# Kernel tuning notes

Measured on AMD Instinct MI355X. Metric: run time of the kernel, lower is better.

## Reference

```python
import jax, jax.numpy as jnp
import numpy as np

N, D, E, OUT = 100000, 128, 600000, 128


def setup_inputs() -> dict:
    key = jax.random.key(0)
    k1, k2, k3, k4, k5 = jax.random.split(key, 5)
    x = jax.random.normal(k1, (N, D), dtype=jnp.float32)
    # Linear params (stored as [in, out]; y = h @ W + b, same math as nn.Linear)
    W = jax.random.normal(k2, (D, OUT), dtype=jnp.float32) * (1.0 / np.sqrt(D))
    b = jax.random.normal(k3, (OUT,), dtype=jnp.float32) * 0.01
    # Flattened ragged neighbor lists as COO edges: node edge_dst[e] aggregates x[edge_src[e]]
    edge_src = jax.random.randint(k4, (E,), 0, N, dtype=jnp.int32)
    edge_dst = jnp.sort(jax.random.randint(k5, (E,), 0, N, dtype=jnp.int32))
    return {"x": x, "W": W, "b": b, "edge_src": edge_src, "edge_dst": edge_dst}


def reference(x, W, b, edge_src, edge_dst):
    n = x.shape[0]
    # segment-mean of neighbor features per destination node
    neigh_sum = jax.ops.segment_sum(x[edge_src], edge_dst, num_segments=n)  # [N, D]
    deg = jax.ops.segment_sum(jnp.ones((edge_dst.shape[0],), x.dtype), edge_dst, num_segments=n)  # [N]
    # nodes with no neighbors keep zero mean (matches `if neigh:` branch)
    neigh_mean = neigh_sum / jnp.maximum(deg, 1.0)[:, None]
    h = x + neigh_mean
    return jax.nn.relu(h @ W + b)
```

## Files before the change

### kernel.cpp

```cpp
#include <hip/hip_runtime.h>
#include <hip/hip_bf16.h>


#define FD  128
#define BR  64
#define HSB 136

typedef __attribute__((ext_vector_type(8))) short bf16x8;
typedef __attribute__((ext_vector_type(4))) float f32x4;

__device__ __forceinline__ short f2bf(float f) {
    unsigned u = __float_as_uint(f);
    unsigned r = (u + 0x7FFFu + ((u >> 16) & 1u)) >> 16;
    return (short)r;
}

__global__ __launch_bounds__(256) void prep_kernel(
    const float* __restrict__ W, const int* __restrict__ edst,
    int* __restrict__ rp, short* __restrict__ pkW, int N, int E)
{
    int gid = blockIdx.x * 256 + threadIdx.x;
    if (gid < E) {
        int cur = edst[gid];
        int prev = gid ? edst[gid - 1] : -1;
        for (int v = prev + 1; v <= cur; ++v) rp[v] = gid;
        if (gid == E - 1)
            for (int v = cur + 1; v <= N; ++v) rp[v] = E;
    }
    if (gid < 2048) {
        int wave = gid >> 9, rem = gid & 511;
        int ct = rem >> 8, rem2 = rem & 255;
        int kt = rem2 >> 6, lane = rem2 & 63;
        int q = lane >> 4, lr = lane & 15;
        int col = wave * 32 + ct * 16 + lr;
        int k0 = kt * 32 + q * 8;
        short tmp[8];
#pragma unroll
        for (int e = 0; e < 8; ++e)
            tmp[e] = f2bf(W[(size_t)(k0 + e) * FD + col]);
        *(bf16x8*)(pkW + (size_t)gid * 8) = *(bf16x8*)tmp;
    }
}

__global__ __launch_bounds__(256) void meanagg_main_kernel(
    const float* __restrict__ x, const short* __restrict__ pkW,
    const float* __restrict__ bias, const int* __restrict__ esrc,
    const int* __restrict__ rp, float* __restrict__ out, int N, int E)
{
    __shared__ short shb[BR * HSB];
    __shared__ int seg[BR + 1];

    const int t = threadIdx.x;
    const int base = blockIdx.x * BR;

    if (t < BR + 1) {
        int idx = base + t;
        seg[t] = rp[idx > N ? N : idx];
    }
    __syncthreads();

    const int wave = t >> 6;
    const int lane = t & 63;
    const int sw = lane >> 5;
    const int sl = lane & 31;
    const int lb = sw << 5;
    const int rowbase = wave * 16;

    {
        int rb0 = rowbase + sw;
        int r0  = base + rb0;
        int s0  = (r0 < N) ? seg[rb0] : 0;
        int e0  = (r0 < N) ? seg[rb0 + 1] : 0;
        int src_next = (s0 + sl < e0) ? esrc[s0 + sl] : 0;
        float4 xv_next = make_float4(0.f, 0.f, 0.f, 0.f);
        if (r0 < N) xv_next = *(const float4*)(x + (size_t)r0 * FD + 4 * sl);

        int s = s0, e = e0;
        for (int it = 0; it < 8; ++it) {
            const int cur_rb = rowbase + it * 2 + sw;
            const int cur_r  = base + cur_rb;
            const int cur_s  = s, cur_e = e;
            const int src_l  = src_next;
            const float4 xv  = xv_next;

            if (it < 7) {
                int nrb = rowbase + (it + 1) * 2 + sw;
                int nr  = base + nrb;
                s = (nr < N) ? seg[nrb] : 0;
                e = (nr < N) ? seg[nrb + 1] : 0;
                src_next = (s + sl < e) ? esrc[s + sl] : 0;
                xv_next = make_float4(0.f, 0.f, 0.f, 0.f);
                if (nr < N) xv_next = *(const float4*)(x + (size_t)nr * FD + 4 * sl);
            }

            if (cur_r < N) {
                float4 a0 = make_float4(0.f, 0.f, 0.f, 0.f), a1 = a0;
                int srcv = src_l;
                for (int cs = cur_s; cs < cur_e; cs += 32) {
                    int m = cur_e - cs; if (m > 32) m = 32;
                    if (cs != cur_s)
                        srcv = (cs + sl < cur_e) ? esrc[cs + sl] : 0;
                    for (int j0 = 0; j0 < m; j0 += 8) {
                        const int rem = m - j0;
                        float4 v[8];
#pragma unroll
                        for (int u = 0; u < 8; ++u) {
                            int idx = __shfl(srcv, lb + ((j0 + u) & 31));
                            v[u] = *(const float4*)(x + (size_t)idx * FD + 4 * sl);
                        }
#pragma unroll
                        for (int u = 0; u < 8; ++u) {
                            float f = (u < rem) ? 1.f : 0.f;
                            float4* A = (u & 1) ? &a1 : &a0;
                            A->x = fmaf(v[u].x, f, A->x);
                            A->y = fmaf(v[u].y, f, A->y);
                            A->z = fmaf(v[u].z, f, A->z);
                            A->w = fmaf(v[u].w, f, A->w);
                        }
                    }
                }
                int deg = cur_e - cur_s;
                float inv = 1.0f / (float)(deg > 0 ? deg : 1);
                short4 hb;
                hb.x = f2bf(xv.x + (a0.x + a1.x) * inv);
                hb.y = f2bf(xv.y + (a0.y + a1.y) * inv);
                hb.z = f2bf(xv.z + (a0.z + a1.z) * inv);
                hb.w = f2bf(xv.w + (a0.w + a1.w) * inv);
                *(short4*)(shb + cur_rb * HSB + 4 * sl) = hb;
            }
        }
    }
    __syncthreads();

    const int lr = lane & 15;
    const int q  = lane >> 4;
    const int colb = wave * 32;

    bf16x8 bfr[2][4];
#pragma unroll
    for (int ct = 0; ct < 2; ++ct)
#pragma unroll
        for (int kt = 0; kt < 4; ++kt) {
            int f = ((wave * 2 + ct) * 4 + kt) * 64 + lane;
            bfr[ct][kt] = *(const bf16x8*)(pkW + (size_t)f * 8);
        }

    f32x4 acc[4][2];
#pragma unroll
    for (int rt = 0; rt < 4; ++rt) {
        acc[rt][0] = (f32x4){0.f, 0.f, 0.f, 0.f};
        acc[rt][1] = (f32x4){0.f, 0.f, 0.f, 0.f};
    }

#pragma unroll
    for (int rt = 0; rt < 4; ++rt)
#pragma unroll
        for (int kt = 0; kt < 4; ++kt) {
            bf16x8 a = *(const bf16x8*)(shb + (rt * 16 + lr) * HSB + kt * 32 + q * 8);
            acc[rt][0] = __builtin_amdgcn_mfma_f32_16x16x32_bf16(a, bfr[0][kt], acc[rt][0], 0, 0, 0);
            acc[rt][1] = __builtin_amdgcn_mfma_f32_16x16x32_bf16(a, bfr[1][kt], acc[rt][1], 0, 0, 0);
        }

    const float b0 = bias[colb + lr];
    const float b1 = bias[colb + 16 + lr];

#pragma unroll
    for (int rt = 0; rt < 4; ++rt)
#pragma unroll
        for (int j = 0; j < 4; ++j) {
            int row = base + rt * 16 + q * 4 + j;
            if (row < N) {
                float v0 = acc[rt][0][j] + b0; v0 = v0 > 0.f ? v0 : 0.f;
                float v1 = acc[rt][1][j] + b1; v1 = v1 > 0.f ? v1 : 0.f;
                out[(size_t)row * FD + colb + lr]      = v0;
                out[(size_t)row * FD + colb + 16 + lr] = v1;
            }
        }
}

__global__ __launch_bounds__(256) void meanagg_fused_kernel(
    const float* __restrict__ x, const float* __restrict__ W,
    const float* __restrict__ bias, const int* __restrict__ esrc,
    const int* __restrict__ edst, float* __restrict__ out, int N, int E)
{
    __shared__ short shb[BR * HSB];
    __shared__ int seg[BR + 1];

    const int t = threadIdx.x;
    const int base = blockIdx.x * BR;

    if (t < BR + 1) {
        int v = base + t;
        int lo = 0, hi = E;
        while (lo < hi) {
            int mid = (lo + hi) >> 1;
            if (edst[mid] < v) lo = mid + 1; else hi = mid;
        }
        seg[t] = lo;
    }
    __syncthreads();

    const int wave = t >> 6;
    const int lane = t & 63;
    const int sw = lane >> 5;
    const int sl = lane & 31;
    const int lb = sw << 5;
    const int rowbase = wave * 16;

    {
        int rb0 = rowbase + sw;
        int r0  = base + rb0;
        int s0  = (r0 < N) ? seg[rb0] : 0;
        int e0  = (r0 < N) ? seg[rb0 + 1] : 0;
        int src_next = (s0 + sl < e0) ? esrc[s0 + sl] : 0;
        float4 xv_next = make_float4(0.f, 0.f, 0.f, 0.f);
        if (r0 < N) xv_next = *(const float4*)(x + (size_t)r0 * FD + 4 * sl);

        int s = s0, e = e0;
        for (int it = 0; it < 8; ++it) {
            const int cur_rb = rowbase + it * 2 + sw;
            const int cur_r  = base + cur_rb;
            const int cur_s  = s, cur_e = e;
            const int src_l  = src_next;
            const float4 xv  = xv_next;

            if (it < 7) {
                int nrb = rowbase + (it + 1) * 2 + sw;
                int nr  = base + nrb;
                s = (nr < N) ? seg[nrb] : 0;
                e = (nr < N) ? seg[nrb + 1] : 0;
                src_next = (s + sl < e) ? esrc[s + sl] : 0;
                xv_next = make_float4(0.f, 0.f, 0.f, 0.f);
                if (nr < N) xv_next = *(const float4*)(x + (size_t)nr * FD + 4 * sl);
            }

            if (cur_r < N) {
                float4 a0 = make_float4(0.f, 0.f, 0.f, 0.f), a1 = a0;
                int srcv = src_l;
                for (int cs = cur_s; cs < cur_e; cs += 32) {
                    int m = cur_e - cs; if (m > 32) m = 32;
                    if (cs != cur_s)
                        srcv = (cs + sl < cur_e) ? esrc[cs + sl] : 0;
                    for (int j0 = 0; j0 < m; j0 += 8) {
                        const int rem = m - j0;
                        float4 v[8];
#pragma unroll
                        for (int u = 0; u < 8; ++u) {
                            int idx = __shfl(srcv, lb + ((j0 + u) & 31));
                            v[u] = *(const float4*)(x + (size_t)idx * FD + 4 * sl);
                        }
#pragma unroll
                        for (int u = 0; u < 8; ++u) {
                            float f = (u < rem) ? 1.f : 0.f;
                            float4* A = (u & 1) ? &a1 : &a0;
                            A->x = fmaf(v[u].x, f, A->x);
                            A->y = fmaf(v[u].y, f, A->y);
                            A->z = fmaf(v[u].z, f, A->z);
                            A->w = fmaf(v[u].w, f, A->w);
                        }
                    }
                }
                int deg = cur_e - cur_s;
                float inv = 1.0f / (float)(deg > 0 ? deg : 1);
                short4 hb;
                hb.x = f2bf(xv.x + (a0.x + a1.x) * inv);
                hb.y = f2bf(xv.y + (a0.y + a1.y) * inv);
                hb.z = f2bf(xv.z + (a0.z + a1.z) * inv);
                hb.w = f2bf(xv.w + (a0.w + a1.w) * inv);
                *(short4*)(shb + cur_rb * HSB + 4 * sl) = hb;
            }
        }
    }
    __syncthreads();

    const int lr = lane & 15;
    const int q  = lane >> 4;
    const int colb = wave * 32;

    bf16x8 bfr[2][4];
#pragma unroll
    for (int ct = 0; ct < 2; ++ct) {
        int col = colb + ct * 16 + lr;
#pragma unroll
        for (int kt = 0; kt < 4; ++kt) {
            bf16x8 f;
#pragma unroll
            for (int e = 0; e < 8; ++e)
                f[e] = f2bf(W[(size_t)(kt * 32 + q * 8 + e) * FD + col]);
            bfr[ct][kt] = f;
        }
    }

    f32x4 acc[4][2];
#pragma unroll
    for (int rt = 0; rt < 4; ++rt) {
        acc[rt][0] = (f32x4){0.f, 0.f, 0.f, 0.f};
        acc[rt][1] = (f32x4){0.f, 0.f, 0.f, 0.f};
    }

#pragma unroll
    for (int rt = 0; rt < 4; ++rt)
#pragma unroll
        for (int kt = 0; kt < 4; ++kt) {
            bf16x8 a = *(const bf16x8*)(shb + (rt * 16 + lr) * HSB + kt * 32 + q * 8);
            acc[rt][0] = __builtin_amdgcn_mfma_f32_16x16x32_bf16(a, bfr[0][kt], acc[rt][0], 0, 0, 0);
            acc[rt][1] = __builtin_amdgcn_mfma_f32_16x16x32_bf16(a, bfr[1][kt], acc[rt][1], 0, 0, 0);
        }

    const float b0 = bias[colb + lr];
    const float b1 = bias[colb + 16 + lr];

#pragma unroll
    for (int rt = 0; rt < 4; ++rt)
#pragma unroll
        for (int j = 0; j < 4; ++j) {
            int row = base + rt * 16 + q * 4 + j;
            if (row < N) {
                float v0 = acc[rt][0][j] + b0; v0 = v0 > 0.f ? v0 : 0.f;
                float v1 = acc[rt][1][j] + b1; v1 = v1 > 0.f ? v1 : 0.f;
                out[(size_t)row * FD + colb + lr]      = v0;
                out[(size_t)row * FD + colb + 16 + lr] = v1;
            }
        }
}

extern "C" void kernel_launch(void* const* d_in, const int* in_sizes, int n_in,
                              void* d_out, int out_size, void* d_ws, size_t ws_size,
                              hipStream_t stream) {
    const float* x    = (const float*)d_in[0];
    const float* W    = (const float*)d_in[1];
    const float* bias = (const float*)d_in[2];
    const int* esrc   = (const int*)d_in[3];
    const int* edst   = (const int*)d_in[4];
    float* out        = (float*)d_out;

    int N = in_sizes[0] / FD;
    int E = in_sizes[3];
    int blocks = (N + BR - 1) / BR;

    size_t rp_bytes  = (size_t)(N + 1) * 4;
    size_t pk_off    = (rp_bytes + 511) & ~(size_t)511;
    size_t need      = pk_off + 2048 * 8 * 2;

    if (ws_size >= need) {
        int* rp    = (int*)d_ws;
        short* pkW = (short*)((char*)d_ws + pk_off);
        int pblocks = (E + 255) / 256;
        prep_kernel<<<pblocks, 256, 0, stream>>>(W, edst, rp, pkW, N, E);
        meanagg_main_kernel<<<blocks, 256, 0, stream>>>(x, pkW, bias, esrc, rp, out, N, E);
    } else {
        meanagg_fused_kernel<<<blocks, 256, 0, stream>>>(x, W, bias, esrc, edst, out, N, E);
    }
}
```

Measured before the change: 71.76 us.

## Pre-convert node features to bf16 and gather bf16 rows in aggregation

Adds a prep pass that converts x to bf16 in workspace alongside the CSR row pointers and packed W. A new main kernel gathers neighbor rows as bf16 (16 lanes × 8 values per row) with 6-wide unrolled loads, which halves the bytes moved by the random gather. The cost is an extra full read of x and a write of its bf16 copy each call, plus reduced precision in the aggregated features. The fallback fused kernel is also simplified, dropping its software prefetch.

```diff
diff --git a/kernel.cpp b/kernel.cpp
--- a/kernel.cpp
+++ b/kernel.cpp
@@ -11,8 +11,194 @@
 
 __device__ __forceinline__ short f2bf(float f) {
     unsigned u = __float_as_uint(f);
-    unsigned r = (u + 0x7FFFu + ((u >> 16) & 1u)) >> 16;
-    return (short)r;
+    return (short)((u + 0x7FFFu + ((u >> 16) & 1u)) >> 16);
+}
+__device__ __forceinline__ float bf2f(short s) {
+    return __uint_as_float(((unsigned)(unsigned short)s) << 16);
+}
+
+__global__ __launch_bounds__(256) void prep_full_kernel(
+    const float* __restrict__ x, const float* __restrict__ W,
+    const int* __restrict__ edst, int* __restrict__ rp,
+    short* __restrict__ pkW, short* __restrict__ xb, int N, int E)
+{
+    const int gid = blockIdx.x * 256 + threadIdx.x;
+    const int nth = gridDim.x * 256;
+
+    const int nv = N * FD / 8;
+    for (int i = gid; i < nv; i += nth) {
+        float4 f0 = *(const float4*)(x + (size_t)i * 8);
+        float4 f1 = *(const float4*)(x + (size_t)i * 8 + 4);
+        short tmp[8] = {f2bf(f0.x), f2bf(f0.y), f2bf(f0.z), f2bf(f0.w),
+                        f2bf(f1.x), f2bf(f1.y), f2bf(f1.z), f2bf(f1.w)};
+        *(bf16x8*)(xb + (size_t)i * 8) = *(bf16x8*)tmp;
+    }
+    for (int e = gid; e < E; e += nth) {
+        int cur = edst[e];
+        int prev = e ? edst[e - 1] : -1;
+        for (int v = prev + 1; v <= cur; ++v) rp[v] = e;
+        if (e == E - 1)
+            for (int v = cur + 1; v <= N; ++v) rp[v] = E;
+    }
+    if (gid < 2048) {
+        int wave = gid >> 9, rem = gid & 511;
+        int ct = rem >> 8, rem2 = rem & 255;
+        int kt = rem2 >> 6, lane = rem2 & 63;
+        int q = lane >> 4, lr = lane & 15;
+        int col = wave * 32 + ct * 16 + lr;
+        int k0 = kt * 32 + q * 8;
+        short tmp[8];
+#pragma unroll
+        for (int e2 = 0; e2 < 8; ++e2)
+            tmp[e2] = f2bf(W[(size_t)(k0 + e2) * FD + col]);
+        *(bf16x8*)(pkW + (size_t)gid * 8) = *(bf16x8*)tmp;
+    }
+}
+
+__global__ __launch_bounds__(256) void meanagg_main2_kernel(
+    const short* __restrict__ xb, const short* __restrict__ pkW,
+    const float* __restrict__ bias, const int* __restrict__ esrc,
+    const int* __restrict__ rp, float* __restrict__ out, int N, int E)
+{
+    __shared__ short shb[BR * HSB];
+    __shared__ int seg[BR + 1];
+
+    const int t = threadIdx.x;
+    const int base = blockIdx.x * BR;
+
+    if (t < BR + 1) {
+        int idx = base + t;
+        seg[t] = rp[idx > N ? N : idx];
+    }
+    __syncthreads();
+
+    const int wave = t >> 6;
+    const int lane = t & 63;
+    const int qw = lane >> 4;
+    const int ql = lane & 15;
+    const int qb = qw << 4;
+    const int rowbase = wave * 16;
+
+    {
+        int rb0 = rowbase + qw;
+        int r0  = base + rb0;
+        int s = (r0 < N) ? seg[rb0] : 0;
+        int e = (r0 < N) ? seg[rb0 + 1] : 0;
+        int srcv_n = (s + ql < e) ? esrc[s + ql] : 0;
+        bf16x8 xv_n = {0, 0, 0, 0, 0, 0, 0, 0};
+        if (r0 < N) xv_n = *(const bf16x8*)(xb + (size_t)r0 * FD + 8 * ql);
+
+        for (int it = 0; it < 4; ++it) {
+            const int cur_rb = rowbase + it * 4 + qw;
+            const int cur_r  = base + cur_rb;
+            const int cs0 = s, ce = e;
+            int srcv = srcv_n;
+            const bf16x8 xv = xv_n;
+
+            if (it < 3) {
+                int nrb = rowbase + (it + 1) * 4 + qw;
+                int nr  = base + nrb;
+                s = (nr < N) ? seg[nrb] : 0;
+                e = (nr < N) ? seg[nrb + 1] : 0;
+                srcv_n = (s + ql < e) ? esrc[s + ql] : 0;
+                bf16x8 z = {0, 0, 0, 0, 0, 0, 0, 0};
+                xv_n = z;
+                if (nr < N) xv_n = *(const bf16x8*)(xb + (size_t)nr * FD + 8 * ql);
+            }
+
+            if (cur_r < N) {
+                float a[8];
+#pragma unroll
+                for (int p = 0; p < 8; ++p) a[p] = 0.f;
+
+                for (int cs = cs0; cs < ce; cs += 16) {
+                    int m = ce - cs; if (m > 16) m = 16;
+                    if (cs != cs0)
+                        srcv = (cs + ql < ce) ? esrc[cs + ql] : 0;
+                    for (int j0 = 0; j0 < m; j0 += 6) {
+                        uint4 v[6];
+#pragma unroll
+                        for (int u = 0; u < 6; ++u) {
+                            int jj = j0 + u;
+                            int idx = __shfl(srcv, qb + (jj & 15));
+                            if (jj >= m) idx = 0;
+                            v[u] = *(const uint4*)(xb + (size_t)idx * FD + 8 * ql);
+                        }
+#pragma unroll
+                        for (int u = 0; u < 6; ++u) {
+                            float f = (j0 + u < m) ? 1.f : 0.f;
+                            unsigned w;
+                            w = v[u].x;
+                            a[0] = fmaf(__uint_as_float(w << 16), f, a[0]);
+                            a[1] = fmaf(__uint_as_float(w & 0xFFFF0000u), f, a[1]);
+                            w = v[u].y;
+                            a[2] = fmaf(__uint_as_float(w << 16), f, a[2]);
+                            a[3] = fmaf(__uint_as_float(w & 0xFFFF0000u), f, a[3]);
+                            w = v[u].z;
+                            a[4] = fmaf(__uint_as_float(w << 16), f, a[4]);
+                            a[5] = fmaf(__uint_as_float(w & 0xFFFF0000u), f, a[5]);
+                            w = v[u].w;
+                            a[6] = fmaf(__uint_as_float(w << 16), f, a[6]);
+                            a[7] = fmaf(__uint_as_float(w & 0xFFFF0000u), f, a[7]);
+                        }
+                    }
+                }
+                int deg = ce - cs0;
+                float inv = 1.0f / (float)(deg > 0 ? deg : 1);
+                short hb[8];
+#pragma unroll
+                for (int p = 0; p < 8; ++p)
+                    hb[p] = f2bf(bf2f(xv[p]) + a[p] * inv);
+                *(bf16x8*)(shb + cur_rb * HSB + 8 * ql) = *(bf16x8*)hb;
+            }
+        }
+    }
+    __syncthreads();
+
+    const int lr = lane & 15;
+    const int q  = lane >> 4;
+    const int colb = wave * 32;
+
+    bf16x8 bfr[2][4];
+#pragma unroll
+    for (int ct = 0; ct < 2; ++ct)
+#pragma unroll
+        for (int kt = 0; kt < 4; ++kt) {
+            int f = ((wave * 2 + ct) * 4 + kt) * 64 + lane;
+            bfr[ct][kt] = *(const bf16x8*)(pkW + (size_t)f * 8);
+        }
+
+    f32x4 acc[4][2];
+#pragma unroll
+    for (int rt = 0; rt < 4; ++rt) {
+        acc[rt][0] = (f32x4){0.f, 0.f, 0.f, 0.f};
+        acc[rt][1] = (f32x4){0.f, 0.f, 0.f, 0.f};
+    }
+
+#pragma unroll
+    for (int rt = 0; rt < 4; ++rt)
+#pragma unroll
+        for (int kt = 0; kt < 4; ++kt) {
+            bf16x8 av = *(const bf16x8*)(shb + (rt * 16 + lr) * HSB + kt * 32 + q * 8);
+            acc[rt][0] = __builtin_amdgcn_mfma_f32_16x16x32_bf16(av, bfr[0][kt], acc[rt][0], 0, 0, 0);
+            acc[rt][1] = __builtin_amdgcn_mfma_f32_16x16x32_bf16(av, bfr[1][kt], acc[rt][1], 0, 0, 0);
+        }
+
+    const float b0 = bias[colb + lr];
+    const float b1 = bias[colb + 16 + lr];
+
+#pragma unroll
+    for (int rt = 0; rt < 4; ++rt)
+#pragma unroll
+        for (int j = 0; j < 4; ++j) {
+            int row = base + rt * 16 + q * 4 + j;
+            if (row < N) {
+                float v0 = acc[rt][0][j] + b0; v0 = v0 > 0.f ? v0 : 0.f;
+                float v1 = acc[rt][1][j] + b1; v1 = v1 > 0.f ? v1 : 0.f;
+                out[(size_t)row * FD + colb + lr]      = v0;
+                out[(size_t)row * FD + colb + 16 + lr] = v1;
+            }
+        }
 }
 
 __global__ __launch_bounds__(256) void prep_kernel(
@@ -156,9 +342,9 @@
     for (int rt = 0; rt < 4; ++rt)
 #pragma unroll
         for (int kt = 0; kt < 4; ++kt) {
-            bf16x8 a = *(const bf16x8*)(shb + (rt * 16 + lr) * HSB + kt * 32 + q * 8);
-            acc[rt][0] = __builtin_amdgcn_mfma_f32_16x16x32_bf16(a, bfr[0][kt], acc[rt][0], 0, 0, 0);
-            acc[rt][1] = __builtin_amdgcn_mfma_f32_16x16x32_bf16(a, bfr[1][kt], acc[rt][1], 0, 0, 0);
+            bf16x8 av = *(const bf16x8*)(shb + (rt * 16 + lr) * HSB + kt * 32 + q * 8);
+            acc[rt][0] = __builtin_amdgcn_mfma_f32_16x16x32_bf16(av, bfr[0][kt], acc[rt][0], 0, 0, 0);
+            acc[rt][1] = __builtin_amdgcn_mfma_f32_16x16x32_bf16(av, bfr[1][kt], acc[rt][1], 0, 0, 0);
         }
 
     const float b0 = bias[colb + lr];
@@ -207,69 +393,39 @@
     const int lb = sw << 5;
     const int rowbase = wave * 16;
 
-    {
-        int rb0 = rowbase + sw;
-        int r0  = base + rb0;
-        int s0  = (r0 < N) ? seg[rb0] : 0;
-        int e0  = (r0 < N) ? seg[rb0 + 1] : 0;
-        int src_next = (s0 + sl < e0) ? esrc[s0 + sl] : 0;
-        float4 xv_next = make_float4(0.f, 0.f, 0.f, 0.f);
-        if (r0 < N) xv_next = *(const float4*)(x + (size_t)r0 * FD + 4 * sl);
-
-        int s = s0, e = e0;
-        for (int it = 0; it < 8; ++it) {
-            const int cur_rb = rowbase + it * 2 + sw;
-            const int cur_r  = base + cur_rb;
-            const int cur_s  = s, cur_e = e;
-            const int src_l  = src_next;
-            const float4 xv  = xv_next;
-
-            if (it < 7) {
-                int nrb = rowbase + (it + 1) * 2 + sw;
-                int nr  = base + nrb;
-                s = (nr < N) ? seg[nrb] : 0;
-                e = (nr < N) ? seg[nrb + 1] : 0;
-                src_next = (s + sl < e) ? esrc[s + sl] : 0;
-                xv_next = make_float4(0.f, 0.f, 0.f, 0.f);
-                if (nr < N) xv_next = *(const float4*)(x + (size_t)nr * FD + 4 * sl);
-            }
-
-            if (cur_r < N) {
-                float4 a0 = make_float4(0.f, 0.f, 0.f, 0.f), a1 = a0;
-                int srcv = src_l;
-                for (int cs = cur_s; cs < cur_e; cs += 32) {
-                    int m = cur_e - cs; if (m > 32) m = 32;
-                    if (cs != cur_s)
-                        srcv = (cs + sl < cur_e) ? esrc[cs + sl] : 0;
-                    for (int j0 = 0; j0 < m; j0 += 8) {
-                        const int rem = m - j0;
-                        float4 v[8];
-#pragma unroll
-                        for (int u = 0; u < 8; ++u) {
-                            int idx = __shfl(srcv, lb + ((j0 + u) & 31));
-                            v[u] = *(const float4*)(x + (size_t)idx * FD + 4 * sl);
-                        }
-#pragma unroll
-                        for (int u = 0; u < 8; ++u) {
-                            float f = (u < rem) ? 1.f : 0.f;
-                            float4* A = (u & 1) ? &a1 : &a0;
-                            A->x = fmaf(v[u].x, f, A->x);
-                            A->y = fmaf(v[u].y, f, A->y);
-                            A->z = fmaf(v[u].z, f, A->z);
-                            A->w = fmaf(v[u].w, f, A->w);
-                        }
-                    }
+    for (int it = 0; it < 8; ++it) {
+        int cur_rb = rowbase + it * 2 + sw;
+        int cur_r  = base + cur_rb;
+        if (cur_r >= N) break;
+        int cur_s = seg[cur_rb], cur_e = seg[cur_rb + 1];
+        float4 a0 = make_float4(0.f, 0.f, 0.f, 0.f), a1 = a0;
+        for (int cs = cur_s; cs < cur_e; cs += 32) {
+            int m = cur_e - cs; if (m > 32) m = 32;
+            int srcv = (cs + sl < cur_e) ? esrc[cs + sl] : 0;
+            for (int j0 = 0; j0 < m; j0 += 8) {
+                const int rem = m - j0;
+#pragma unroll
+                for (int u = 0; u < 8; ++u) {
+                    int idx = __shfl(srcv, lb + ((j0 + u) & 31));
+                    float4 v = *(const float4*)(x + (size_t)idx * FD + 4 * sl);
+                    float f = (u < rem) ? 1.f : 0.f;
+                    float4* A = (u & 1) ? &a1 : &a0;
+                    A->x = fmaf(v.x, f, A->x);
+                    A->y = fmaf(v.y, f, A->y);
+                    A->z = fmaf(v.z, f, A->z);
+                    A->w = fmaf(v.w, f, A->w);
                 }
-                int deg = cur_e - cur_s;
-                float inv = 1.0f / (float)(deg > 0 ? deg : 1);
-                short4 hb;
-                hb.x = f2bf(xv.x + (a0.x + a1.x) * inv);
-                hb.y = f2bf(xv.y + (a0.y + a1.y) * inv);
-                hb.z = f2bf(xv.z + (a0.z + a1.z) * inv);
-                hb.w = f2bf(xv.w + (a0.w + a1.w) * inv);
-                *(short4*)(shb + cur_rb * HSB + 4 * sl) = hb;
-            }
-        }
+            }
+        }
+        float4 xv = *(const float4*)(x + (size_t)cur_r * FD + 4 * sl);
+        int deg = cur_e - cur_s;
+        float inv = 1.0f / (float)(deg > 0 ? deg : 1);
+        short4 hb;
+        hb.x = f2bf(xv.x + (a0.x + a1.x) * inv);
+        hb.y = f2bf(xv.y + (a0.y + a1.y) * inv);
+        hb.z = f2bf(xv.z + (a0.z + a1.z) * inv);
+        hb.w = f2bf(xv.w + (a0.w + a1.w) * inv);
+        *(short4*)(shb + cur_rb * HSB + 4 * sl) = hb;
     }
     __syncthreads();
 
@@ -302,9 +458,9 @@
     for (int rt = 0; rt < 4; ++rt)
 #pragma unroll
         for (int kt = 0; kt < 4; ++kt) {
-            bf16x8 a = *(const bf16x8*)(shb + (rt * 16 + lr) * HSB + kt * 32 + q * 8);
-            acc[rt][0] = __builtin_amdgcn_mfma_f32_16x16x32_bf16(a, bfr[0][kt], acc[rt][0], 0, 0, 0);
-            acc[rt][1] = __builtin_amdgcn_mfma_f32_16x16x32_bf16(a, bfr[1][kt], acc[rt][1], 0, 0, 0);
+            bf16x8 av = *(const bf16x8*)(shb + (rt * 16 + lr) * HSB + kt * 32 + q * 8);
+            acc[rt][0] = __builtin_amdgcn_mfma_f32_16x16x32_bf16(av, bfr[0][kt], acc[rt][0], 0, 0, 0);
+            acc[rt][1] = __builtin_amdgcn_mfma_f32_16x16x32_bf16(av, bfr[1][kt], acc[rt][1], 0, 0, 0);
         }
 
     const float b0 = bias[colb + lr];
@@ -338,11 +494,19 @@
     int E = in_sizes[3];
     int blocks = (N + BR - 1) / BR;
 
-    size_t rp_bytes  = (size_t)(N + 1) * 4;
-    size_t pk_off    = (rp_bytes + 511) & ~(size_t)511;
-    size_t need      = pk_off + 2048 * 8 * 2;
-
-    if (ws_size >= need) {
+    size_t rp_bytes = (size_t)(N + 1) * 4;
+    size_t pk_off   = (rp_bytes + 511) & ~(size_t)511;
+    size_t xb_off   = (pk_off + 2048 * 8 * 2 + 511) & ~(size_t)511;
+    size_t need_med = pk_off + 2048 * 8 * 2;
+    size_t need_big = xb_off + (size_t)N * FD * 2;
+
+    if (ws_size >= need_big) {
+        int* rp    = (int*)d_ws;
+        short* pkW = (short*)((char*)d_ws + pk_off);
+        short* xb  = (short*)((char*)d_ws + xb_off);
+        prep_full_kernel<<<2048, 256, 0, stream>>>(x, W, edst, rp, pkW, xb, N, E);
+        meanagg_main2_kernel<<<blocks, 256, 0, stream>>>(xb, pkW, bias, esrc, rp, out, N, E);
+    } else if (ws_size >= need_med) {
         int* rp    = (int*)d_ws;
         short* pkW = (short*)((char*)d_ws + pk_off);
         int pblocks = (E + 255) / 256;
```

New measurement: 57.65 us. 1.24x faster.
